# Kernel optimization log

Measured on AMD Instinct MI355X. Metric: run time of the kernel, lower is better.

The kernel has to match this reference:

```python
import jax, jax.numpy as jnp
import numpy as np

B, S, D = 16, 2048, 128

def setup_inputs() -> dict:
    key = jax.random.key(0)
    kq, kk, kv, km = jax.random.split(key, 4)
    Q = jax.random.normal(kq, (B, S, D), dtype=jnp.float32)
    K = jax.random.normal(kk, (B, S, D), dtype=jnp.float32)
    V = jax.random.normal(kv, (B, S, D), dtype=jnp.float32)
    # mask: True entries are masked out (filled with -inf), same as torch.masked_fill_
    mask = jax.random.randint(km, (B, S, S), 0, 2).astype(bool)
    return {"Q": Q, "K": K, "V": V, "mask": mask, "dk": 128}

def reference(Q, K, V, mask, dk):
    # scores: [B, S_q, S_k]
    w = jnp.einsum('bqd,bkd->bqk', Q, K)
    w = jnp.where(mask, -jnp.inf, w)
    # scale applied to masked scores (as in original: mask first, then divide);
    # -inf / scale stays -inf, so math matches exactly.
    scale = jnp.asarray(dk, w.dtype) ** 0.5
    p = jax.nn.softmax(w / scale, axis=-1)
    # context: [B, S_q, D]
    return jnp.einsum('bqk,bkd->bqd', p, V)
```

## Files before the change

kernel.cpp:

```cpp
#include <hip/hip_runtime.h>
#include <hip/hip_bf16.h>
#include <stdint.h>

typedef __attribute__((ext_vector_type(8))) short short8;
typedef __attribute__((ext_vector_type(4))) float floatx4;

#define S_LEN 2048
#define DH    128
#define BQ    64
#define BKV   64
#define NSTEP (S_LEN / BKV)
#define SCALE 0.08838834764831845f

__device__ __forceinline__ unsigned short f2b(float f) {
    union { float f; unsigned u; } v; v.f = f;
    unsigned r = v.u + 0x7fffu + ((v.u >> 16) & 1u);
    return (unsigned short)(r >> 16);
}

__device__ __forceinline__ unsigned cvt_pk(float lo, float hi) {
    unsigned r;
    asm("v_cvt_pk_bf16_f32 %0, %1, %2" : "=v"(r) : "v"(lo), "v"(hi));
    return r;
}

__device__ __forceinline__ void gll16(const void* g, void* l) {
    __builtin_amdgcn_global_load_lds(
        (__attribute__((address_space(1))) void*)(g),
        (__attribute__((address_space(3))) void*)(l), 16, 0, 0);
}


__global__ __launch_bounds__(256) void conv_k(const float* __restrict__ K,
                                              unsigned short* __restrict__ Kbf)
{
    int i = blockIdx.x * 256 + threadIdx.x;
    float4 v = ((const float4*)K)[i];
    ushort4 o;
    o.x = f2b(v.x); o.y = f2b(v.y); o.z = f2b(v.z); o.w = f2b(v.w);
    ((ushort4*)Kbf)[i] = o;
}

__global__ __launch_bounds__(256) void transp_v(const float* __restrict__ V,
                                                unsigned short* __restrict__ Vt)
{
    __shared__ float t[32][33];
    const int k0 = blockIdx.x * 32, d0 = blockIdx.y * 32, b = blockIdx.z;
    const int tx = threadIdx.x & 31, ty = threadIdx.x >> 5;
    const float* Vb = V + ((size_t)b * S_LEN + k0) * DH + d0;
    #pragma unroll
    for (int i = 0; i < 4; ++i)
        t[ty + 8 * i][tx] = Vb[(size_t)(ty + 8 * i) * DH + tx];
    __syncthreads();
    unsigned short* Vtb = Vt + ((size_t)b * DH + d0) * S_LEN + k0;
    #pragma unroll
    for (int i = 0; i < 4; ++i)
        Vtb[(size_t)(ty + 8 * i) * S_LEN + tx] = f2b(t[tx][ty + 8 * i]);
}

#define LDS_BYTES 59392

__global__ __launch_bounds__(256, 3)
void attn_fwd(const float* __restrict__ Q, const unsigned short* __restrict__ Kbf,
              const unsigned short* __restrict__ Vt, const int* __restrict__ M,
              float* __restrict__ O)
{
    __shared__ __align__(128) char lds[LDS_BYTES];

    const int tid  = threadIdx.x;
    const int lane = tid & 63;
    const int w    = tid >> 6;
    const int c    = lane & 15;
    const int g    = lane >> 4;
    const int qt   = blockIdx.x;
    const int b    = blockIdx.y;
    const int q0   = qt * BQ;

    const int vd = tid & 127;
    const int vh = tid >> 7;
    const int krow_l = lane >> 4;
    const int kcol_l = (lane & 15) * 16;

    short8 qf[4];
    {
        const float* qrow = Q + ((size_t)(b * S_LEN + q0 + w * 16 + c)) * DH;
        #pragma unroll
        for (int dk = 0; dk < 4; ++dk) {
            const float* p = qrow + dk * 32 + g * 8;
            float4 a  = *(const float4*)(p);
            float4 bb = *(const float4*)(p + 4);
            short8 f;
            f[0] = f2b(a.x * SCALE);  f[1] = f2b(a.y * SCALE);
            f[2] = f2b(a.z * SCALE);  f[3] = f2b(a.w * SCALE);
            f[4] = f2b(bb.x * SCALE); f[5] = f2b(bb.y * SCALE);
            f[6] = f2b(bb.z * SCALE); f[7] = f2b(bb.w * SCALE);
            qf[dk] = f;
        }
    }

    float m_run = -1e30f;
    float l_run = 0.f;
    floatx4 accO[8];
    #pragma unroll
    for (int i = 0; i < 8; ++i) accO[i] = (floatx4)(0.f);

    const char*           Kb8 = (const char*)(Kbf + (size_t)b * S_LEN * DH);
    const unsigned short* Vtb = Vt + (size_t)b * DH * S_LEN;
    const int* Mrow = M + (size_t)b * S_LEN * S_LEN
                        + (size_t)(q0 + w * 16 + c) * S_LEN + 4 * g;

    short8 vreg[4];
    int4   mregA[4], mregB[4];
    char*  psw = lds + 51200 + w * 2048;

#define LOAD_MASK(DST, TT) {                                                  \
    const int* mp_ = Mrow + (TT) * BKV;                                       \
    DST[0] = *(const int4*)(mp_);                                             \
    DST[1] = *(const int4*)(mp_ + 16);                                        \
    DST[2] = *(const int4*)(mp_ + 32);                                        \
    DST[3] = *(const int4*)(mp_ + 48); }

    #pragma unroll
    for (int i = 0; i < 4; ++i) {
        int j = (w << 2) | i;
        int r = 4 * j + krow_l;
        unsigned cb = (unsigned)kcol_l ^ (unsigned)((r & 7) << 4);
        gll16(Kb8 + (size_t)r * 256 + cb, lds + j * 1024);
    }
    #pragma unroll
    for (int j = 0; j < 4; ++j)
        vreg[j] = *(const short8*)(Vtb + (size_t)vd * S_LEN + vh * 32 + j * 8);
    LOAD_MASK(mregA, 0);
    LOAD_MASK(mregB, 1);
    __syncthreads();

#define STEP_BODY(T, MCUR) {                                                  \
    const int pb  = (T) & 1;                                                  \
    const int kv0 = (T) * BKV;                                                \
                 \
    if ((T) + 1 < NSTEP) {                                                    \
        const char* Ksrc = Kb8 + (size_t)(kv0 + BKV) * 256;                   \
        char* KHn = lds + ((pb ^ 1) * 16384);                                 \
        _Pragma("unroll")                                                     \
        for (int i = 0; i < 4; ++i) {                                         \
            int j = (w << 2) | i;                                             \
            int r = 4 * j + krow_l;                                           \
            unsigned cb = (unsigned)kcol_l ^ (unsigned)((r & 7) << 4);        \
            gll16(Ksrc + (size_t)r * 256 + cb, KHn + j * 1024);               \
        }                                                                     \
    }                                                                         \
                                           \
    _Pragma("unroll")                                                         \
    for (int j = 0; j < 4; ++j)                                               \
        *(short8*)(lds + 32768 + vd * 144 + vh * 64 + j * 16) = vreg[j];      \
                                             \
    if ((T) + 1 < NSTEP) {                                                    \
        const unsigned short* vs_ = Vtb + (size_t)vd * S_LEN                  \
                                   + (kv0 + BKV) + vh * 32;                   \
        _Pragma("unroll")                                                     \
        for (int j = 0; j < 4; ++j)                                           \
            vreg[j] = *(const short8*)(vs_ + j * 8);                          \
    }                                                                         \
                         \
    floatx4 accS[4];                                                          \
    _Pragma("unroll")                                                         \
    for (int n = 0; n < 4; ++n) accS[n] = (floatx4)(0.f);                     \
    {                                                                         \
        const char* KHp = lds + pb * 16384;                                   \
        _Pragma("unroll")                                                     \
        for (int n = 0; n < 4; ++n) {                                         \
            const char* krow = KHp + (n * 16 + c) * 256;                      \
            _Pragma("unroll")                                                 \
            for (int dk = 0; dk < 4; ++dk) {                                  \
                short8 kf = *(const short8*)(krow +                           \
                    ((unsigned)(dk * 64 + g * 16) ^ (unsigned)((c & 7) << 4)));\
                accS[n] = __builtin_amdgcn_mfma_f32_16x16x32_bf16(            \
                              kf, qf[dk], accS[n], 0, 0, 0);                  \
            }                                                                 \
        }                                                                     \
    }                                                                         \
             \
    float p_[4][4];                                                           \
    _Pragma("unroll")                                                         \
    for (int n = 0; n < 4; ++n) {                                             \
        int4 mm = MCUR[n];                                                    \
        p_[n][0] = mm.x ? -1e30f : accS[n][0];                                \
        p_[n][1] = mm.y ? -1e30f : accS[n][1];                                \
        p_[n][2] = mm.z ? -1e30f : accS[n][2];                                \
        p_[n][3] = mm.w ? -1e30f : accS[n][3];                                \
    }                                                                         \
    float mx = p_[0][0];                                                      \
    _Pragma("unroll")                                                         \
    for (int n = 0; n < 4; ++n)                                               \
        _Pragma("unroll")                                                     \
        for (int r = 0; r < 4; ++r) mx = fmaxf(mx, p_[n][r]);                 \
    mx = fmaxf(mx, __shfl_xor(mx, 16));                                       \
    mx = fmaxf(mx, __shfl_xor(mx, 32));                                       \
    float mn   = fmaxf(m_run, mx);                                            \
    float corr = __expf(m_run - mn);                                          \
    m_run = mn;                                                               \
    float ts = 0.f;                                                           \
    _Pragma("unroll")                                                         \
    for (int n = 0; n < 4; ++n)                                               \
        _Pragma("unroll")                                                     \
        for (int r = 0; r < 4; ++r) {                                         \
            p_[n][r] = __expf(p_[n][r] - mn);                                 \
            ts += p_[n][r];                                                   \
        }                                                                     \
    ts += __shfl_xor(ts, 16);                                                 \
    ts += __shfl_xor(ts, 32);                                                 \
    l_run = l_run * corr + ts;                                                \
                             \
    if ((T) + 2 < NSTEP) LOAD_MASK(MCUR, (T) + 2);                            \
               \
    _Pragma("unroll")                                                         \
    for (int n = 0; n < 4; ++n) {                                             \
        unsigned w0 = cvt_pk(p_[n][0], p_[n][1]);                             \
        unsigned w1 = cvt_pk(p_[n][2], p_[n][3]);                             \
        unsigned long long pk = (unsigned long long)w0                        \
                              | ((unsigned long long)w1 << 32);               \
        *(unsigned long long*)(psw + (4 * n + g) * 128                        \
                               + ((c * 8) ^ (g << 3))) = pk;                  \
    }                                                                         \
                                     \
    _Pragma("unroll")                                                         \
    for (int s8 = 0; s8 < 8; ++s8) {                                          \
        floatx4 o = accO[s8];                                                 \
        o[0] *= corr; o[1] *= corr; o[2] *= corr; o[3] *= corr;               \
        accO[s8] = o;                                                         \
    }                                                                         \
                                    \
    asm volatile("s_waitcnt lgkmcnt(0)" ::: "memory");                        \
    __builtin_amdgcn_s_barrier();                                             \
                                              \
    _Pragma("unroll")                                                         \
    for (int sub = 0; sub < 2; ++sub) {                                       \
        int ra = 8 * sub + 2 * g;                                             \
        unsigned long long lo = *(const unsigned long long*)(psw + ra * 128   \
                                + ((c * 8) ^ ((ra & 3) << 3)));               \
        unsigned long long hi = *(const unsigned long long*)(psw + (ra+1)*128 \
                                + ((c * 8) ^ (((ra + 1) & 3) << 3)));         \
        union { unsigned long long q[2]; short8 v; } pu;                      \
        pu.q[0] = lo; pu.q[1] = hi;                                           \
        short8 pf = pu.v;                                                     \
        _Pragma("unroll")                                                     \
        for (int s8 = 0; s8 < 8; ++s8) {                                      \
            short8 vf = *(const short8*)(lds + 32768 + (s8 * 16 + c) * 144    \
                                         + sub * 64 + g * 16);                \
            accO[s8] = __builtin_amdgcn_mfma_f32_16x16x32_bf16(               \
                           vf, pf, accO[s8], 0, 0, 0);                        \
        }                                                                     \
    }                                                                         \
                                                               \
    __syncthreads(); }

    for (int t = 0; t < NSTEP; t += 2) {
        STEP_BODY(t,     mregA)
        STEP_BODY(t + 1, mregB)
    }
#undef STEP_BODY
#undef LOAD_MASK

    float inv = (l_run > 0.f) ? 1.f / l_run : 0.f;
    float* Ob = O + ((size_t)(b * S_LEN + q0 + w * 16 + c)) * DH;
    #pragma unroll
    for (int s8 = 0; s8 < 8; ++s8) {
        float4 ov;
        ov.x = accO[s8][0] * inv; ov.y = accO[s8][1] * inv;
        ov.z = accO[s8][2] * inv; ov.w = accO[s8][3] * inv;
        *(float4*)(Ob + s8 * 16 + 4 * g) = ov;
    }
}

#define FB_LDS_BYTES 77824

__global__ __launch_bounds__(256, 2)
void attn_fwd_fb(const float* __restrict__ Q, const float* __restrict__ K,
                 const float* __restrict__ V, const int* __restrict__ M,
                 float* __restrict__ O)
{
    __shared__ __align__(128) char lds[FB_LDS_BYTES];

    const int tid  = threadIdx.x;
    const int lane = tid & 63;
    const int w    = tid >> 6;
    const int c    = lane & 15;
    const int g    = lane >> 4;
    const int qt   = blockIdx.x;
    const int b    = blockIdx.y;
    const int q0   = qt * BQ;

    const int rbase = tid >> 5;
    const int c4    = tid & 31;
    const unsigned swk = (unsigned)(c4 * 8) ^ (unsigned)(rbase << 4);
    const int vd    = tid & 127;
    const int vk0   = (tid >> 7) * 32;

    short8 qf[4];
    {
        const float* qrow = Q + ((size_t)(b * S_LEN + q0 + w * 16 + c)) * DH;
        #pragma unroll
        for (int dk = 0; dk < 4; ++dk) {
            const float* p = qrow + dk * 32 + g * 8;
            float4 a  = *(const float4*)(p);
            float4 bb = *(const float4*)(p + 4);
            short8 f;
            f[0] = f2b(a.x * SCALE);  f[1] = f2b(a.y * SCALE);
            f[2] = f2b(a.z * SCALE);  f[3] = f2b(a.w * SCALE);
            f[4] = f2b(bb.x * SCALE); f[5] = f2b(bb.y * SCALE);
            f[6] = f2b(bb.z * SCALE); f[7] = f2b(bb.w * SCALE);
            qf[dk] = f;
        }
    }

    float m_run[4] = {-1e30f, -1e30f, -1e30f, -1e30f};
    float l_run[4] = {0.f, 0.f, 0.f, 0.f};
    floatx4 accO[8];
    #pragma unroll
    for (int i = 0; i < 8; ++i) accO[i] = (floatx4)(0.f);

    const float* Kb = K + (size_t)b * S_LEN * DH;
    const float* Vb = V + (size_t)b * S_LEN * DH;
    const int*   Mb = M + (size_t)b * S_LEN * S_LEN + (size_t)q0 * S_LEN;

    size_t moff[4];
    #pragma unroll
    for (int r = 0; r < 4; ++r)
        moff[r] = (size_t)(w * 16 + 4 * g + r) * S_LEN;

    float4 kreg[8];
    float  vreg[32];
    int    mreg[16];

    #pragma unroll
    for (int i = 0; i < 8; ++i)
        kreg[i] = *(const float4*)(Kb + (size_t)(i * 8 + rbase) * DH + c4 * 4);
    #pragma unroll
    for (int j = 0; j < 32; ++j)
        vreg[j] = Vb[(size_t)(vk0 + j) * DH + vd];
    #pragma unroll
    for (int r = 0; r < 4; ++r)
        #pragma unroll
        for (int n = 0; n < 4; ++n)
            mreg[r * 4 + n] = Mb[moff[r] + n * 16 + c];

    #pragma unroll
    for (int i = 0; i < 8; ++i) {
        float4 kv = kreg[i];
        unsigned long long kp =
              (unsigned long long)f2b(kv.x)
            | ((unsigned long long)f2b(kv.y) << 16)
            | ((unsigned long long)f2b(kv.z) << 32)
            | ((unsigned long long)f2b(kv.w) << 48);
        *(unsigned long long*)(lds + (i * 8 + rbase) * 256 + swk) = kp;
    }
    {
        char* vbase = lds + 32768 + vd * 144 + vk0 * 2;
        #pragma unroll
        for (int i = 0; i < 4; ++i) {
            short8 pk;
            #pragma unroll
            for (int e = 0; e < 8; ++e) pk[e] = f2b(vreg[i * 8 + e]);
            *(short8*)(vbase + i * 16) = pk;
        }
    }
    #pragma unroll
    for (int i = 0; i < 8; ++i)
        kreg[i] = *(const float4*)(Kb + (size_t)(BKV + i * 8 + rbase) * DH + c4 * 4);
    #pragma unroll
    for (int j = 0; j < 32; ++j)
        vreg[j] = Vb[(size_t)(BKV + vk0 + j) * DH + vd];

    __syncthreads();

    char* psw = lds + 69632 + w * 2048;

    for (int step = 0; step < NSTEP; ++step) {
        const int p = step & 1;
        const int kv0 = step * BKV;
        char* KHp = lds + p * 16384;
        char* VTp = lds + 32768 + p * 18432;

        floatx4 accS[4];
        #pragma unroll
        for (int n = 0; n < 4; ++n) accS[n] = (floatx4)(0.f);
        #pragma unroll
        for (int n = 0; n < 4; ++n) {
            const char* krow = KHp + (n * 16 + c) * 256;
            #pragma unroll
            for (int dk = 0; dk < 4; ++dk) {
                unsigned colb = (unsigned)(dk * 64 + g * 16) ^ (unsigned)((c & 7) << 4);
                short8 kf = *(const short8*)(krow + colb);
                accS[n] = __builtin_amdgcn_mfma_f32_16x16x32_bf16(qf[dk], kf, accS[n], 0, 0, 0);
            }
        }

        float pv[4][4];
        float corr[4];
        #pragma unroll
        for (int r = 0; r < 4; ++r) {
            float sv[4];
            #pragma unroll
            for (int n = 0; n < 4; ++n) {
                float s = accS[n][r];
                if (mreg[r * 4 + n]) s = -1e30f;
                sv[n] = s;
            }
            float tm = fmaxf(fmaxf(sv[0], sv[1]), fmaxf(sv[2], sv[3]));
            #pragma unroll
            for (int off = 1; off < 16; off <<= 1)
                tm = fmaxf(tm, __shfl_xor(tm, off, 64));
            float mn = fmaxf(m_run[r], tm);
            corr[r]  = __expf(m_run[r] - mn);
            m_run[r] = mn;
            float ts = 0.f;
            #pragma unroll
            for (int n = 0; n < 4; ++n) { pv[n][r] = __expf(sv[n] - mn); ts += pv[n][r]; }
            #pragma unroll
            for (int off = 1; off < 16; off <<= 1)
                ts += __shfl_xor(ts, off, 64);
            l_run[r] = l_run[r] * corr[r] + ts;
        }
        if (step + 1 < NSTEP) {
            const int kvn = kv0 + BKV;
            #pragma unroll
            for (int r = 0; r < 4; ++r)
                #pragma unroll
                for (int n = 0; n < 4; ++n)
                    mreg[r * 4 + n] = Mb[moff[r] + kvn + n * 16 + c];
        }

        #pragma unroll
        for (int s8 = 0; s8 < 8; ++s8) {
            floatx4 o = accO[s8];
            o[0] *= corr[0]; o[1] *= corr[1]; o[2] *= corr[2]; o[3] *= corr[3];
            accO[s8] = o;
        }

        #pragma unroll
        for (int r = 0; r < 4; ++r) {
            int rl = 4 * g + r;
            #pragma unroll
            for (int n = 0; n < 4; ++n) {
                unsigned colb = (unsigned)((n * 16 + c) * 2) ^ (unsigned)((rl & 7) << 4);
                *(unsigned short*)(psw + rl * 128 + colb) = f2b(pv[n][r]);
            }
        }

        #pragma unroll
        for (int sub = 0; sub < 2; ++sub) {
            unsigned colb = (unsigned)(sub * 64 + g * 16) ^ (unsigned)((c & 7) << 4);
            short8 pf = *(const short8*)(psw + c * 128 + colb);
            #pragma unroll
            for (int s8 = 0; s8 < 8; ++s8) {
                short8 vf = *(const short8*)(VTp + (s8 * 16 + c) * 144 + sub * 64 + g * 16);
                accO[s8] = __builtin_amdgcn_mfma_f32_16x16x32_bf16(pf, vf, accO[s8], 0, 0, 0);
            }
        }

        if (step + 1 < NSTEP) {
            char* KHn = lds + (p ^ 1) * 16384;
            char* VTn = lds + 32768 + (p ^ 1) * 18432;
            #pragma unroll
            for (int i = 0; i < 8; ++i) {
                float4 kv = kreg[i];
                unsigned long long kp =
                      (unsigned long long)f2b(kv.x)
                    | ((unsigned long long)f2b(kv.y) << 16)
                    | ((unsigned long long)f2b(kv.z) << 32)
                    | ((unsigned long long)f2b(kv.w) << 48);
                *(unsigned long long*)(KHn + (i * 8 + rbase) * 256 + swk) = kp;
            }
            char* vbase = VTn + vd * 144 + vk0 * 2;
            #pragma unroll
            for (int i = 0; i < 4; ++i) {
                short8 pk;
                #pragma unroll
                for (int e = 0; e < 8; ++e) pk[e] = f2b(vreg[i * 8 + e]);
                *(short8*)(vbase + i * 16) = pk;
            }
            if (step + 2 < NSTEP) {
                const int kvn2 = kv0 + 2 * BKV;
                #pragma unroll
                for (int i = 0; i < 8; ++i)
                    kreg[i] = *(const float4*)(Kb + (size_t)(kvn2 + i * 8 + rbase) * DH + c4 * 4);
                #pragma unroll
                for (int j = 0; j < 32; ++j)
                    vreg[j] = Vb[(size_t)(kvn2 + vk0 + j) * DH + vd];
            }
        }
        __syncthreads();
    }

    float inv[4];
    #pragma unroll
    for (int r = 0; r < 4; ++r) inv[r] = (l_run[r] > 0.f) ? 1.f / l_run[r] : 0.f;
    float* Ob = O + ((size_t)(b * S_LEN + q0 + w * 16)) * DH;
    #pragma unroll
    for (int s8 = 0; s8 < 8; ++s8) {
        #pragma unroll
        for (int r = 0; r < 4; ++r) {
            Ob[(size_t)(4 * g + r) * DH + s8 * 16 + c] = accO[s8][r] * inv[r];
        }
    }
}

extern "C" void kernel_launch(void* const* d_in, const int* in_sizes, int n_in,
                              void* d_out, int out_size, void* d_ws, size_t ws_size,
                              hipStream_t stream) {
    const float* Q = (const float*)d_in[0];
    const float* K = (const float*)d_in[1];
    const float* V = (const float*)d_in[2];
    const int*   M = (const int*)d_in[3];
    float*       O = (float*)d_out;

    const size_t elems = (size_t)16 * S_LEN * DH;
    if (ws_size >= 2 * elems * sizeof(unsigned short)) {
        unsigned short* Kbf = (unsigned short*)d_ws;
        unsigned short* Vt  = (unsigned short*)d_ws + elems;
        conv_k<<<dim3((unsigned)(elems / 4 / 256)), dim3(256), 0, stream>>>(K, Kbf);
        transp_v<<<dim3(S_LEN / 32, DH / 32, 16), dim3(256), 0, stream>>>(V, Vt);
        attn_fwd<<<dim3(S_LEN / BQ, 16), dim3(256), 0, stream>>>(Q, Kbf, Vt, M, O);
    } else {
        attn_fwd_fb<<<dim3(S_LEN / BQ, 16), dim3(256), 0, stream>>>(Q, K, V, M, O);
    }
}
```

Before: 121.6 us.

## Double-buffer V tile, drop mid-step barrier, use exp2 with lazy rescale

```diff
diff --git a/kernel.cpp b/kernel.cpp
--- a/kernel.cpp
+++ b/kernel.cpp
@@ -11,6 +11,10 @@
 #define BKV   64
 #define NSTEP (S_LEN / BKV)
 #define SCALE 0.08838834764831845f
+#define SCALE2 0.12753785429791905f
+#define DTHR 11.541560327111708f
+
+__device__ __forceinline__ float ex2(float x) { return __builtin_amdgcn_exp2f(x); }
 
 __device__ __forceinline__ unsigned short f2b(float f) {
     union { float f; unsigned u; } v; v.f = f;
@@ -58,9 +62,9 @@
         Vtb[(size_t)(ty + 8 * i) * S_LEN + tx] = f2b(t[tx][ty + 8 * i]);
 }
 
-#define LDS_BYTES 59392
-
-__global__ __launch_bounds__(256, 3)
+#define LDS_BYTES 77824
+
+__global__ __launch_bounds__(256, 2)
 void attn_fwd(const float* __restrict__ Q, const unsigned short* __restrict__ Kbf,
               const unsigned short* __restrict__ Vt, const int* __restrict__ M,
               float* __restrict__ O)
@@ -80,6 +84,241 @@
     const int vh = tid >> 7;
     const int krow_l = lane >> 4;
     const int kcol_l = (lane & 15) * 16;
+
+    short8 qf[4];
+    {
+        const float* qrow = Q + ((size_t)(b * S_LEN + q0 + w * 16 + c)) * DH;
+        #pragma unroll
+        for (int dk = 0; dk < 4; ++dk) {
+            const float* p = qrow + dk * 32 + g * 8;
+            float4 a  = *(const float4*)(p);
+            float4 bb = *(const float4*)(p + 4);
+            short8 f;
+            f[0] = f2b(a.x * SCALE2);  f[1] = f2b(a.y * SCALE2);
+            f[2] = f2b(a.z * SCALE2);  f[3] = f2b(a.w * SCALE2);
+            f[4] = f2b(bb.x * SCALE2); f[5] = f2b(bb.y * SCALE2);
+            f[6] = f2b(bb.z * SCALE2); f[7] = f2b(bb.w * SCALE2);
+            qf[dk] = f;
+        }
+    }
+
+    float m_run = -1e30f;
+    float l_run = 0.f;
+    floatx4 accO[8];
+    #pragma unroll
+    for (int i = 0; i < 8; ++i) accO[i] = (floatx4)(0.f);
+
+    const char*           Kb8 = (const char*)(Kbf + (size_t)b * S_LEN * DH);
+    const unsigned short* Vtb = Vt + (size_t)b * DH * S_LEN;
+    const int* Mrow = M + (size_t)b * S_LEN * S_LEN
+                        + (size_t)(q0 + w * 16 + c) * S_LEN + 4 * g;
+
+    short8 vreg[4];
+    int4   mregA[4], mregB[4];
+    char*  psw = lds + 69632 + w * 2048;
+
+#define LOAD_MASK(DST, TT) {                                                  \
+    const int* mp_ = Mrow + (TT) * BKV;                                       \
+    DST[0] = *(const int4*)(mp_);                                             \
+    DST[1] = *(const int4*)(mp_ + 16);                                        \
+    DST[2] = *(const int4*)(mp_ + 32);                                        \
+    DST[3] = *(const int4*)(mp_ + 48); }
+
+    #pragma unroll
+    for (int i = 0; i < 4; ++i) {
+        int j = (w << 2) | i;
+        int r = 4 * j + krow_l;
+        unsigned cb = (unsigned)kcol_l ^ (unsigned)((r & 7) << 4);
+        gll16(Kb8 + (size_t)r * 256 + cb, lds + j * 1024);
+    }
+    #pragma unroll
+    for (int j = 0; j < 4; ++j)
+        vreg[j] = *(const short8*)(Vtb + (size_t)vd * S_LEN + vh * 32 + j * 8);
+    #pragma unroll
+    for (int j = 0; j < 4; ++j)
+        *(short8*)(lds + 32768 + vd * 144 + vh * 64 + j * 16) = vreg[j];
+    #pragma unroll
+    for (int j = 0; j < 4; ++j)
+        vreg[j] = *(const short8*)(Vtb + (size_t)vd * S_LEN + BKV + vh * 32 + j * 8);
+    LOAD_MASK(mregA, 0);
+    LOAD_MASK(mregB, 1);
+    __syncthreads();
+
+#define STEP_BODY(T, MCUR) {                                                  \
+    const int pb  = (T) & 1;                                                  \
+    const int kv0 = (T) * BKV;                                                \
+                 \
+    if ((T) + 1 < NSTEP) {                                                    \
+        const char* Ksrc = Kb8 + (size_t)(kv0 + BKV) * 256;                   \
+        char* KHn = lds + ((pb ^ 1) * 16384);                                 \
+        _Pragma("unroll")                                                     \
+        for (int i = 0; i < 4; ++i) {                                         \
+            int j = (w << 2) | i;                                             \
+            int r = 4 * j + krow_l;                                           \
+            unsigned cb = (unsigned)kcol_l ^ (unsigned)((r & 7) << 4);        \
+            gll16(Ksrc + (size_t)r * 256 + cb, KHn + j * 1024);               \
+        }                                                                     \
+    }                                                                         \
+                                       \
+    if ((T) + 1 < NSTEP) {                                                    \
+        _Pragma("unroll")                                                     \
+        for (int j = 0; j < 4; ++j)                                           \
+            *(short8*)(lds + 32768 + (pb ^ 1) * 18432 + vd * 144 + vh * 64    \
+                       + j * 16) = vreg[j];                                   \
+    }                                                                         \
+                                                     \
+    if ((T) + 2 < NSTEP) {                                                    \
+        const unsigned short* vs_ = Vtb + (size_t)vd * S_LEN                  \
+                                   + (kv0 + 2 * BKV) + vh * 32;               \
+        _Pragma("unroll")                                                     \
+        for (int j = 0; j < 4; ++j)                                           \
+            vreg[j] = *(const short8*)(vs_ + j * 8);                          \
+    }                                                                         \
+                               \
+    floatx4 accS[4];                                                          \
+    _Pragma("unroll")                                                         \
+    for (int n = 0; n < 4; ++n) accS[n] = (floatx4)(0.f);                     \
+    {                                                                         \
+        const char* KHp = lds + pb * 16384;                                   \
+        __builtin_amdgcn_s_setprio(1);                                        \
+        _Pragma("unroll")                                                     \
+        for (int n = 0; n < 4; ++n) {                                         \
+            const char* krow = KHp + (n * 16 + c) * 256;                      \
+            _Pragma("unroll")                                                 \
+            for (int dk = 0; dk < 4; ++dk) {                                  \
+                short8 kf = *(const short8*)(krow +                           \
+                    ((unsigned)(dk * 64 + g * 16) ^ (unsigned)((c & 7) << 4)));\
+                accS[n] = __builtin_amdgcn_mfma_f32_16x16x32_bf16(            \
+                              kf, qf[dk], accS[n], 0, 0, 0);                  \
+            }                                                                 \
+        }                                                                     \
+        __builtin_amdgcn_s_setprio(0);                                        \
+    }                                                                         \
+                                \
+    float p_[4][4];                                                           \
+    _Pragma("unroll")                                                         \
+    for (int n = 0; n < 4; ++n) {                                             \
+        int4 mm = MCUR[n];                                                    \
+        p_[n][0] = mm.x ? -1e30f : accS[n][0];                                \
+        p_[n][1] = mm.y ? -1e30f : accS[n][1];                                \
+        p_[n][2] = mm.z ? -1e30f : accS[n][2];                                \
+        p_[n][3] = mm.w ? -1e30f : accS[n][3];                                \
+    }                                                                         \
+    float mx = p_[0][0];                                                      \
+    _Pragma("unroll")                                                         \
+    for (int n = 0; n < 4; ++n)                                               \
+        _Pragma("unroll")                                                     \
+        for (int r = 0; r < 4; ++r) mx = fmaxf(mx, p_[n][r]);                 \
+    mx = fmaxf(mx, __shfl_xor(mx, 16));                                       \
+    mx = fmaxf(mx, __shfl_xor(mx, 32));                                       \
+    int need = __any(mx - m_run > DTHR);                                      \
+    float corr = 1.0f;                                                        \
+    if (need) {                                                               \
+        float mn = fmaxf(m_run, mx);                                          \
+        corr = ex2(m_run - mn);                                               \
+        m_run = mn;                                                           \
+    }                                                                         \
+    float ts = 0.f;                                                           \
+    _Pragma("unroll")                                                         \
+    for (int n = 0; n < 4; ++n)                                               \
+        _Pragma("unroll")                                                     \
+        for (int r = 0; r < 4; ++r) {                                         \
+            p_[n][r] = ex2(p_[n][r] - m_run);                                 \
+            ts += p_[n][r];                                                   \
+        }                                                                     \
+    ts += __shfl_xor(ts, 16);                                                 \
+    ts += __shfl_xor(ts, 32);                                                 \
+    if (need) {                                                               \
+        l_run = l_run * corr + ts;                                            \
+        _Pragma("unroll")                                                     \
+        for (int s8 = 0; s8 < 8; ++s8) {                                      \
+            floatx4 o = accO[s8];                                             \
+            o[0] *= corr; o[1] *= corr; o[2] *= corr; o[3] *= corr;           \
+            accO[s8] = o;                                                     \
+        }                                                                     \
+    } else {                                                                  \
+        l_run += ts;                                                          \
+    }                                                                         \
+                                                       \
+    if ((T) + 2 < NSTEP) LOAD_MASK(MCUR, (T) + 2);                            \
+                \
+    _Pragma("unroll")                                                         \
+    for (int n = 0; n < 4; ++n) {                                             \
+        unsigned w0 = cvt_pk(p_[n][0], p_[n][1]);                             \
+        unsigned w1 = cvt_pk(p_[n][2], p_[n][3]);                             \
+        unsigned long long pk = (unsigned long long)w0                        \
+                              | ((unsigned long long)w1 << 32);               \
+        *(unsigned long long*)(psw + (4 * n + g) * 128                        \
+                               + ((c * 8) ^ (g << 3))) = pk;                  \
+    }                                                                         \
+                     \
+    {                                                                         \
+        const char* VTp = lds + 32768 + pb * 18432;                           \
+        _Pragma("unroll")                                                     \
+        for (int sub = 0; sub < 2; ++sub) {                                   \
+            int ra = 8 * sub + 2 * g;                                         \
+            unsigned long long lo = *(const unsigned long long*)(psw + ra*128 \
+                                    + ((c * 8) ^ ((ra & 3) << 3)));           \
+            unsigned long long hi = *(const unsigned long long*)(psw          \
+                                    + (ra + 1) * 128                          \
+                                    + ((c * 8) ^ (((ra + 1) & 3) << 3)));     \
+            union { unsigned long long q[2]; short8 v; } pu;                  \
+            pu.q[0] = lo; pu.q[1] = hi;                                       \
+            short8 pf = pu.v;                                                 \
+            __builtin_amdgcn_s_setprio(1);                                    \
+            _Pragma("unroll")                                                 \
+            for (int s8 = 0; s8 < 8; ++s8) {                                  \
+                short8 vf = *(const short8*)(VTp + (s8 * 16 + c) * 144        \
+                                             + sub * 64 + g * 16);            \
+                accO[s8] = __builtin_amdgcn_mfma_f32_16x16x32_bf16(           \
+                               vf, pf, accO[s8], 0, 0, 0);                    \
+            }                                                                 \
+            __builtin_amdgcn_s_setprio(0);                                    \
+        }                                                                     \
+    }                                                                         \
+    __syncthreads(); }
+
+    for (int t = 0; t < NSTEP; t += 2) {
+        STEP_BODY(t,     mregA)
+        STEP_BODY(t + 1, mregB)
+    }
+#undef STEP_BODY
+#undef LOAD_MASK
+
+    float inv = (l_run > 0.f) ? 1.f / l_run : 0.f;
+    float* Ob = O + ((size_t)(b * S_LEN + q0 + w * 16 + c)) * DH;
+    #pragma unroll
+    for (int s8 = 0; s8 < 8; ++s8) {
+        float4 ov;
+        ov.x = accO[s8][0] * inv; ov.y = accO[s8][1] * inv;
+        ov.z = accO[s8][2] * inv; ov.w = accO[s8][3] * inv;
+        *(float4*)(Ob + s8 * 16 + 4 * g) = ov;
+    }
+}
+
+#define FB_LDS_BYTES 77824
+
+__global__ __launch_bounds__(256, 2)
+void attn_fwd_fb(const float* __restrict__ Q, const float* __restrict__ K,
+                 const float* __restrict__ V, const int* __restrict__ M,
+                 float* __restrict__ O)
+{
+    __shared__ __align__(128) char lds[FB_LDS_BYTES];
+
+    const int tid  = threadIdx.x;
+    const int lane = tid & 63;
+    const int w    = tid >> 6;
+    const int c    = lane & 15;
+    const int g    = lane >> 4;
+    const int qt   = blockIdx.x;
+    const int b    = blockIdx.y;
+    const int q0   = qt * BQ;
+
+    const int rbase = tid >> 5;
+    const int c4    = tid & 31;
+    const unsigned swk = (unsigned)(c4 * 8) ^ (unsigned)(rbase << 4);
+    const int vd    = tid & 127;
+    const int vk0   = (tid >> 7) * 32;
 
     short8 qf[4];
     {
@@ -98,221 +337,6 @@
         }
     }
 
-    float m_run = -1e30f;
-    float l_run = 0.f;
-    floatx4 accO[8];
-    #pragma unroll
-    for (int i = 0; i < 8; ++i) accO[i] = (floatx4)(0.f);
-
-    const char*           Kb8 = (const char*)(Kbf + (size_t)b * S_LEN * DH);
-    const unsigned short* Vtb = Vt + (size_t)b * DH * S_LEN;
-    const int* Mrow = M + (size_t)b * S_LEN * S_LEN
-                        + (size_t)(q0 + w * 16 + c) * S_LEN + 4 * g;
-
-    short8 vreg[4];
-    int4   mregA[4], mregB[4];
-    char*  psw = lds + 51200 + w * 2048;
-
-#define LOAD_MASK(DST, TT) {                                                  \
-    const int* mp_ = Mrow + (TT) * BKV;                                       \
-    DST[0] = *(const int4*)(mp_);                                             \
-    DST[1] = *(const int4*)(mp_ + 16);                                        \
-    DST[2] = *(const int4*)(mp_ + 32);                                        \
-    DST[3] = *(const int4*)(mp_ + 48); }
-
-    #pragma unroll
-    for (int i = 0; i < 4; ++i) {
-        int j = (w << 2) | i;
-        int r = 4 * j + krow_l;
-        unsigned cb = (unsigned)kcol_l ^ (unsigned)((r & 7) << 4);
-        gll16(Kb8 + (size_t)r * 256 + cb, lds + j * 1024);
-    }
-    #pragma unroll
-    for (int j = 0; j < 4; ++j)
-        vreg[j] = *(const short8*)(Vtb + (size_t)vd * S_LEN + vh * 32 + j * 8);
-    LOAD_MASK(mregA, 0);
-    LOAD_MASK(mregB, 1);
-    __syncthreads();
-
-#define STEP_BODY(T, MCUR) {                                                  \
-    const int pb  = (T) & 1;                                                  \
-    const int kv0 = (T) * BKV;                                                \
-                 \
-    if ((T) + 1 < NSTEP) {                                                    \
-        const char* Ksrc = Kb8 + (size_t)(kv0 + BKV) * 256;                   \
-        char* KHn = lds + ((pb ^ 1) * 16384);                                 \
-        _Pragma("unroll")                                                     \
-        for (int i = 0; i < 4; ++i) {                                         \
-            int j = (w << 2) | i;                                             \
-            int r = 4 * j + krow_l;                                           \
-            unsigned cb = (unsigned)kcol_l ^ (unsigned)((r & 7) << 4);        \
-            gll16(Ksrc + (size_t)r * 256 + cb, KHn + j * 1024);               \
-        }                                                                     \
-    }                                                                         \
-                                           \
-    _Pragma("unroll")                                                         \
-    for (int j = 0; j < 4; ++j)                                               \
-        *(short8*)(lds + 32768 + vd * 144 + vh * 64 + j * 16) = vreg[j];      \
-                                             \
-    if ((T) + 1 < NSTEP) {                                                    \
-        const unsigned short* vs_ = Vtb + (size_t)vd * S_LEN                  \
-                                   + (kv0 + BKV) + vh * 32;                   \
-        _Pragma("unroll")                                                     \
-        for (int j = 0; j < 4; ++j)                                           \
-            vreg[j] = *(const short8*)(vs_ + j * 8);                          \
-    }                                                                         \
-                         \
-    floatx4 accS[4];                                                          \
-    _Pragma("unroll")                                                         \
-    for (int n = 0; n < 4; ++n) accS[n] = (floatx4)(0.f);                     \
-    {                                                                         \
-        const char* KHp = lds + pb * 16384;                                   \
-        _Pragma("unroll")                                                     \
-        for (int n = 0; n < 4; ++n) {                                         \
-            const char* krow = KHp + (n * 16 + c) * 256;                      \
-            _Pragma("unroll")                                                 \
-            for (int dk = 0; dk < 4; ++dk) {                                  \
-                short8 kf = *(const short8*)(krow +                           \
-                    ((unsigned)(dk * 64 + g * 16) ^ (unsigned)((c & 7) << 4)));\
-                accS[n] = __builtin_amdgcn_mfma_f32_16x16x32_bf16(            \
-                              kf, qf[dk], accS[n], 0, 0, 0);                  \
-            }                                                                 \
-        }                                                                     \
-    }                                                                         \
-             \
-    float p_[4][4];                                                           \
-    _Pragma("unroll")                                                         \
-    for (int n = 0; n < 4; ++n) {                                             \
-        int4 mm = MCUR[n];                                                    \
-        p_[n][0] = mm.x ? -1e30f : accS[n][0];                                \
-        p_[n][1] = mm.y ? -1e30f : accS[n][1];                                \
-        p_[n][2] = mm.z ? -1e30f : accS[n][2];                                \
-        p_[n][3] = mm.w ? -1e30f : accS[n][3];                                \
-    }                                                                         \
-    float mx = p_[0][0];                                                      \
-    _Pragma("unroll")                                                         \
-    for (int n = 0; n < 4; ++n)                                               \
-        _Pragma("unroll")                                                     \
-        for (int r = 0; r < 4; ++r) mx = fmaxf(mx, p_[n][r]);                 \
-    mx = fmaxf(mx, __shfl_xor(mx, 16));                                       \
-    mx = fmaxf(mx, __shfl_xor(mx, 32));                                       \
-    float mn   = fmaxf(m_run, mx);                                            \
-    float corr = __expf(m_run - mn);                                          \
-    m_run = mn;                                                               \
-    float ts = 0.f;                                                           \
-    _Pragma("unroll")                                                         \
-    for (int n = 0; n < 4; ++n)                                               \
-        _Pragma("unroll")                                                     \
-        for (int r = 0; r < 4; ++r) {                                         \
-            p_[n][r] = __expf(p_[n][r] - mn);                                 \
-            ts += p_[n][r];                                                   \
-        }                                                                     \
-    ts += __shfl_xor(ts, 16);                                                 \
-    ts += __shfl_xor(ts, 32);                                                 \
-    l_run = l_run * corr + ts;                                                \
-                             \
-    if ((T) + 2 < NSTEP) LOAD_MASK(MCUR, (T) + 2);                            \
-               \
-    _Pragma("unroll")                                                         \
-    for (int n = 0; n < 4; ++n) {                                             \
-        unsigned w0 = cvt_pk(p_[n][0], p_[n][1]);                             \
-        unsigned w1 = cvt_pk(p_[n][2], p_[n][3]);                             \
-        unsigned long long pk = (unsigned long long)w0                        \
-                              | ((unsigned long long)w1 << 32);               \
-        *(unsigned long long*)(psw + (4 * n + g) * 128                        \
-                               + ((c * 8) ^ (g << 3))) = pk;                  \
-    }                                                                         \
-                                     \
-    _Pragma("unroll")                                                         \
-    for (int s8 = 0; s8 < 8; ++s8) {                                          \
-        floatx4 o = accO[s8];                                                 \
-        o[0] *= corr; o[1] *= corr; o[2] *= corr; o[3] *= corr;               \
-        accO[s8] = o;                                                         \
-    }                                                                         \
-                                    \
-    asm volatile("s_waitcnt lgkmcnt(0)" ::: "memory");                        \
-    __builtin_amdgcn_s_barrier();                                             \
-                                              \
-    _Pragma("unroll")                                                         \
-    for (int sub = 0; sub < 2; ++sub) {                                       \
-        int ra = 8 * sub + 2 * g;                                             \
-        unsigned long long lo = *(const unsigned long long*)(psw + ra * 128   \
-                                + ((c * 8) ^ ((ra & 3) << 3)));               \
-        unsigned long long hi = *(const unsigned long long*)(psw + (ra+1)*128 \
-                                + ((c * 8) ^ (((ra + 1) & 3) << 3)));         \
-        union { unsigned long long q[2]; short8 v; } pu;                      \
-        pu.q[0] = lo; pu.q[1] = hi;                                           \
-        short8 pf = pu.v;                                                     \
-        _Pragma("unroll")                                                     \
-        for (int s8 = 0; s8 < 8; ++s8) {                                      \
-            short8 vf = *(const short8*)(lds + 32768 + (s8 * 16 + c) * 144    \
-                                         + sub * 64 + g * 16);                \
-            accO[s8] = __builtin_amdgcn_mfma_f32_16x16x32_bf16(               \
-                           vf, pf, accO[s8], 0, 0, 0);                        \
-        }                                                                     \
-    }                                                                         \
-                                                               \
-    __syncthreads(); }
-
-    for (int t = 0; t < NSTEP; t += 2) {
-        STEP_BODY(t,     mregA)
-        STEP_BODY(t + 1, mregB)
-    }
-#undef STEP_BODY
-#undef LOAD_MASK
-
-    float inv = (l_run > 0.f) ? 1.f / l_run : 0.f;
-    float* Ob = O + ((size_t)(b * S_LEN + q0 + w * 16 + c)) * DH;
-    #pragma unroll
-    for (int s8 = 0; s8 < 8; ++s8) {
-        float4 ov;
-        ov.x = accO[s8][0] * inv; ov.y = accO[s8][1] * inv;
-        ov.z = accO[s8][2] * inv; ov.w = accO[s8][3] * inv;
-        *(float4*)(Ob + s8 * 16 + 4 * g) = ov;
-    }
-}
-
-#define FB_LDS_BYTES 77824
-
-__global__ __launch_bounds__(256, 2)
-void attn_fwd_fb(const float* __restrict__ Q, const float* __restrict__ K,
-                 const float* __restrict__ V, const int* __restrict__ M,
-                 float* __restrict__ O)
-{
-    __shared__ __align__(128) char lds[FB_LDS_BYTES];
-
-    const int tid  = threadIdx.x;
-    const int lane = tid & 63;
-    const int w    = tid >> 6;
-    const int c    = lane & 15;
-    const int g    = lane >> 4;
-    const int qt   = blockIdx.x;
-    const int b    = blockIdx.y;
-    const int q0   = qt * BQ;
-
-    const int rbase = tid >> 5;
-    const int c4    = tid & 31;
-    const unsigned swk = (unsigned)(c4 * 8) ^ (unsigned)(rbase << 4);
-    const int vd    = tid & 127;
-    const int vk0   = (tid >> 7) * 32;
-
-    short8 qf[4];
-    {
-        const float* qrow = Q + ((size_t)(b * S_LEN + q0 + w * 16 + c)) * DH;
-        #pragma unroll
-        for (int dk = 0; dk < 4; ++dk) {
-            const float* p = qrow + dk * 32 + g * 8;
-            float4 a  = *(const float4*)(p);
-            float4 bb = *(const float4*)(p + 4);
-            short8 f;
-            f[0] = f2b(a.x * SCALE);  f[1] = f2b(a.y * SCALE);
-            f[2] = f2b(a.z * SCALE);  f[3] = f2b(a.w * SCALE);
-            f[4] = f2b(bb.x * SCALE); f[5] = f2b(bb.y * SCALE);
-            f[6] = f2b(bb.z * SCALE); f[7] = f2b(bb.w * SCALE);
-            qf[dk] = f;
-        }
-    }
-
     float m_run[4] = {-1e30f, -1e30f, -1e30f, -1e30f};
     float l_run[4] = {0.f, 0.f, 0.f, 0.f};
     floatx4 accO[8];
```

Result: faster. 115.5 us (-5.0%).
